# Optimization experiments

Hardware: AMD Instinct MI355X
Metric: run time of the kernel (lower is better)

Reference implementation:

```python
import jax, jax.numpy as jnp
import numpy as np

DIM, NH, HD = 1536, 12, 128          # dim, num_heads, head_dim
F, H, W = 100, 8, 8                   # video grid; F>81 triggers frame-sparse branch
L = F * H * W                         # 6400 tokens


def setup_inputs() -> dict:
    key = jax.random.key(0)
    ks = jax.random.split(key, 8)
    lin = lambda k: jax.random.normal(k, (DIM, DIM), jnp.float32) * 0.02
    return {
        "x": jax.random.normal(ks[0], (1, L, DIM), jnp.float32),
        "freqs": jax.random.uniform(ks[1], (1024, HD // 2), jnp.float32, 0.0, 2.0 * np.pi),
        "Wq": lin(ks[2]), "bq": jnp.zeros((DIM,), jnp.float32),
        "Wk": lin(ks[3]), "bk": jnp.zeros((DIM,), jnp.float32),
        "Wv": lin(ks[4]), "bv": jnp.zeros((DIM,), jnp.float32),
        "Wo": lin(ks[5]), "bo": jnp.zeros((DIM,), jnp.float32),
        "gq": jnp.ones((DIM,), jnp.float32),
        "gk": jnp.ones((DIM,), jnp.float32),
        "seq_lens": jnp.full((1,), L, jnp.int32),
        "grid_sizes": jnp.array([[F, H, W]], jnp.int32),
    }


def _rms(x, g, eps=1e-6):
    # WanRMSNorm: rms over the full channel dim, fp32 math
    m = jnp.mean(x * x, axis=-1, keepdims=True)
    return x * jax.lax.rsqrt(m + eps) * g


def _rope_tables(freqs, f, h, w):
    # freqs: [1024, c] rope angles; split c into (c-2*(c//3), c//3, c//3) for F/H/W axes
    c = freqs.shape[1]
    c1 = c - 2 * (c // 3)
    c2 = c // 3
    af = jnp.broadcast_to(freqs[:f, None, None, :c1], (f, h, w, c1))
    ah = jnp.broadcast_to(freqs[None, :h, None, c1:c1 + c2], (f, h, w, c2))
    aw = jnp.broadcast_to(freqs[None, None, :w, c1 + c2:], (f, h, w, c2))
    ang = jnp.concatenate([af, ah, aw], axis=-1).reshape(f * h * w, 1, c)  # [L,1,c]
    return jnp.cos(ang), jnp.sin(ang)


def _rope_apply(x, cos, sin):
    # x: [B,L,n,d]; pairs (real, imag) interleaved along d -> complex rotation
    b, l, n, d = x.shape
    xr, xi = x[..., 0::2], x[..., 1::2]                       # [B,L,n,c]
    out_r = xr * cos - xi * sin
    out_i = xr * sin + xi * cos
    return jnp.stack([out_r, out_i], axis=-1).reshape(b, l, n, d)


def reference(x, freqs, Wq, bq, Wk, bk, Wv, bv, Wo, bo, gq, gk, seq_lens, grid_sizes):
    b, l, _ = x.shape
    n, d = NH, HD
    f, h, w = [int(v) for v in np.asarray(grid_sizes)[0]]
    q = _rms(x @ Wq + bq, gq).reshape(b, l, n, d)
    k = _rms(x @ Wk + bk, gk).reshape(b, l, n, d)
    v = (x @ Wv + bv).reshape(b, l, n, d)
    cos, sin = _rope_tables(freqs, f, h, w)
    q = _rope_apply(q, cos, sin)
    k = _rope_apply(k, cos, sin)
    if f > 81:  # long-video frame-sparse branch: keep every 2nd frame's K/V tokens
        tpf = h * w
        idx = (jnp.arange(0, f, 2)[:, None] * tpf + jnp.arange(tpf)[None, :]).reshape(-1)
        k = k[:, idx]
        v = v[:, idx]
    # attention in low precision (original uses fp16/bf16), softmax accum fp32
    qb, kb, vb = (t.astype(jnp.bfloat16) for t in (q, k, v))
    scale = 1.0 / np.sqrt(d)
    scores = jnp.einsum('blnd,bknd->bnlk', qb, kb).astype(jnp.float32) * scale
    att = jax.nn.softmax(scores, axis=-1).astype(jnp.bfloat16)
    out = jnp.einsum('bnlk,bknd->blnd', att, vb).reshape(b, l, n * d).astype(jnp.float32)
    return out @ Wo + bo
```

## Files before the change

### kernel.cpp

```cpp
#include <hip/hip_runtime.h>
#include <stdint.h>

typedef unsigned short u16;
typedef short short8 __attribute__((ext_vector_type(8)));
typedef float f32x4 __attribute__((ext_vector_type(4)));
typedef u16 u16x8 __attribute__((ext_vector_type(8)));

#define DIMN 1536
#define LQ   6400
#define LKV  3200
#define NHEAD 12
#define HDIM  128

__device__ __forceinline__ u16 f2bf(float f) {
  uint32_t u = __builtin_bit_cast(uint32_t, f);
  u += 0x7fffu + ((u >> 16) & 1u);
  return (u16)(u >> 16);
}
__device__ __forceinline__ float bf2f(u16 h) {
  uint32_t u = ((uint32_t)h) << 16;
  return __builtin_bit_cast(float, u);
}
__device__ __forceinline__ void async16(const void* g, void* l) {
  __builtin_amdgcn_global_load_lds((const __attribute__((address_space(1))) void*)g,
                                   (__attribute__((address_space(3))) void*)l, 16, 0, 0);
}
#define MFMA16(a, b, c) __builtin_amdgcn_mfma_f32_16x16x32_bf16((a), (b), (c), 0, 0, 0)

__global__ void __launch_bounds__(256) convert_x(const float* __restrict__ x, u16* __restrict__ xb) {
  size_t i = ((size_t)blockIdx.x * 256 + threadIdx.x) * 4;
  float4 v = *(const float4*)(x + i);
  union { u16 h[4]; uint2 u; } p;
  p.h[0] = f2bf(v.x); p.h[1] = f2bf(v.y); p.h[2] = f2bf(v.z); p.h[3] = f2bf(v.w);
  *(uint2*)(xb + i) = p.u;
}

__global__ void __launch_bounds__(256) transpose_w(const float* __restrict__ Wq, const float* __restrict__ Wk,
                                                   const float* __restrict__ Wv, const float* __restrict__ Wo,
                                                   u16* __restrict__ wt) {
  int z = blockIdx.z;
  const float* W = (z == 0) ? Wq : (z == 1) ? Wk : (z == 2) ? Wv : Wo;
  u16* dst = wt + (size_t)z * DIMN * DIMN;
  __shared__ float tile[64][65];
  int c0 = blockIdx.x * 64, r0 = blockIdx.y * 64;
  int t = threadIdx.x;
  int rr = t >> 4, cc = (t & 15) * 4;
#pragma unroll
  for (int j = 0; j < 4; j++) {
    float4 v = *(const float4*)(W + (size_t)(r0 + rr + j * 16) * DIMN + c0 + cc);
    tile[rr + j * 16][cc + 0] = v.x; tile[rr + j * 16][cc + 1] = v.y;
    tile[rr + j * 16][cc + 2] = v.z; tile[rr + j * 16][cc + 3] = v.w;
  }
  __syncthreads();
  int nn = t >> 2, kk = (t & 3) * 16;
  u16x8 a, b;
#pragma unroll
  for (int q = 0; q < 8; q++) a[q] = f2bf(tile[kk + q][nn]);
#pragma unroll
  for (int q = 0; q < 8; q++) b[q] = f2bf(tile[kk + 8 + q][nn]);
  u16* o = dst + (size_t)(c0 + nn) * DIMN + r0 + kk;
  *(u16x8*)(o) = a;
  *(u16x8*)(o + 8) = b;
}

__device__ __forceinline__ void gemm_tile(const u16* __restrict__ A, const u16* __restrict__ Bt,
                                          int m0, int n0, u16* sA, u16* sB, f32x4 acc[4][4]) {
  const int tid = threadIdx.x;
  const int wid = tid >> 6, lane = tid & 63;
  const int wm = wid >> 1, wn = wid & 1;
  const int l15 = lane & 15, quad = lane >> 4;
  const int lrow = lane >> 3;
  const int sgrp = (lane & 7) ^ lrow;
#pragma unroll
  for (int i = 0; i < 4; i++)
#pragma unroll
    for (int j = 0; j < 4; j++) acc[i][j] = f32x4{0.f, 0.f, 0.f, 0.f};
  const u16* ga = A  + (size_t)(m0 + wid * 32 + lrow) * DIMN + sgrp * 8;
  const u16* gb = Bt + (size_t)(n0 + wid * 32 + lrow) * DIMN + sgrp * 8;
  u16* la = sA + (wid * 32) * 64;
  u16* lb = sB + (wid * 32) * 64;
  const int swz = l15 & 7;
  for (int k0 = 0; k0 < DIMN; k0 += 64) {
    __syncthreads();
#pragma unroll
    for (int j = 0; j < 4; j++) async16(ga + k0 + j * 8 * DIMN, la + j * 8 * 64);
#pragma unroll
    for (int j = 0; j < 4; j++) async16(gb + k0 + j * 8 * DIMN, lb + j * 8 * 64);
    __syncthreads();
#pragma unroll
    for (int kk = 0; kk < 64; kk += 32) {
      short8 af[4], bf[4];
#pragma unroll
      for (int s = 0; s < 4; s++)
        af[s] = *(const short8*)(sA + (wm * 64 + s * 16 + l15) * 64 + ((((kk >> 3) + quad) ^ swz) << 3));
#pragma unroll
      for (int s = 0; s < 4; s++)
        bf[s] = *(const short8*)(sB + (wn * 64 + s * 16 + l15) * 64 + ((((kk >> 3) + quad) ^ swz) << 3));
#pragma unroll
      for (int i = 0; i < 4; i++)
#pragma unroll
        for (int j = 0; j < 4; j++) acc[i][j] = MFMA16(af[i], bf[j], acc[i][j]);
    }
  }
}

__global__ void __launch_bounds__(256) gemm_qkv(const u16* __restrict__ xb, const u16* __restrict__ wt,
                                                const float* __restrict__ bq, const float* __restrict__ bk,
                                                const float* __restrict__ bv,
                                                u16* __restrict__ qb, u16* __restrict__ kb, u16* __restrict__ vtb) {
  __shared__ u16 sA[128 * 64];
  __shared__ u16 sB[128 * 64];
  int z = blockIdx.z;
  const u16* Bt = wt + (size_t)z * DIMN * DIMN;
  int m0 = blockIdx.x * 128, n0 = blockIdx.y * 128;
  f32x4 acc[4][4];
  gemm_tile(xb, Bt, m0, n0, sA, sB, acc);
  const float* bias = (z == 0) ? bq : (z == 1) ? bk : bv;
  int tid = threadIdx.x, wid = tid >> 6, lane = tid & 63;
  int wm = wid >> 1, wn = wid & 1, l15 = lane & 15, quad = lane >> 4;
#pragma unroll
  for (int sn = 0; sn < 4; sn++) {
    int c = n0 + wn * 64 + sn * 16 + l15;
    float bb = bias[c];
    int h = c >> 7, d = c & 127;
#pragma unroll
    for (int sm = 0; sm < 4; sm++) {
      int rl = wm * 64 + sm * 16 + quad * 4;
#pragma unroll
      for (int r = 0; r < 4; r++) {
        float val = acc[sm][sn][r] + bb;
        int row = m0 + rl + r;
        if (z == 0) {
          qb[((size_t)h * LQ + row) * HDIM + d] = f2bf(val);
        } else if ((rl + r) < 64) {
          int lk = (row >> 7) * 64 + (row & 63);
          if (z == 1) kb[((size_t)h * LKV + lk) * HDIM + d] = f2bf(val);
          else        vtb[((size_t)h * HDIM + d) * LKV + lk] = f2bf(val);
        }
      }
    }
  }
}

__global__ void __launch_bounds__(256) rms_rope(u16* __restrict__ qb, u16* __restrict__ kb,
                                                const float* __restrict__ freqs,
                                                const float* __restrict__ gq, const float* __restrict__ gk) {
  int t = blockIdx.x * 4 + (threadIdx.x >> 6);
  int lane = threadIdx.x & 63;
  bool isQ = t < LQ;
  int tok = isQ ? t : t - LQ;
  int Lt = isQ ? LQ : LKV;
  u16* buf = isQ ? qb : kb;
  const float* g = isQ ? gq : gk;
  int l = isQ ? tok : ((tok >> 6) * 128 + (tok & 63));
  float a[12], b[12];
  float ss = 0.f;
#pragma unroll
  for (int n = 0; n < NHEAD; n++) {
    ushort2 p = *(const ushort2*)(buf + ((size_t)n * Lt + tok) * HDIM + 2 * lane);
    a[n] = bf2f(p.x); b[n] = bf2f(p.y);
    ss += a[n] * a[n] + b[n] * b[n];
  }
#pragma unroll
  for (int off = 32; off; off >>= 1) ss += __shfl_xor(ss, off);
  float rs = rsqrtf(ss * (1.0f / 1536.0f) + 1e-6f);
  int i = lane;
  int fi = (i < 22) ? (l >> 6) : (i < 43) ? ((l >> 3) & 7) : (l & 7);
  float ang = freqs[fi * 64 + i];
  float sn, cs;
  sincosf(ang, &sn, &cs);
#pragma unroll
  for (int n = 0; n < NHEAD; n++) {
    float2 gg = *(const float2*)(g + n * HDIM + 2 * lane);
    float xr = a[n] * rs * gg.x;
    float xi = b[n] * rs * gg.y;
    ushort2 o;
    o.x = f2bf(xr * cs - xi * sn);
    o.y = f2bf(xr * sn + xi * cs);
    *(ushort2*)(buf + ((size_t)n * Lt + tok) * HDIM + 2 * lane) = o;
  }
}

__global__ void __launch_bounds__(256, 2) attn(const u16* __restrict__ qb, const u16* __restrict__ kb,
                                               const u16* __restrict__ vtb, u16* __restrict__ ob) {
  __shared__ u16 Ks[128 * 128];
  __shared__ u16 Vs[128 * 128];
  int x8 = blockIdx.x & 7, gsl = blockIdx.x >> 3;
  int w = x8 * 75 + gsl;
  int h = w / 50, qt = w % 50;
  int tid = threadIdx.x, wid = tid >> 6, lane = tid & 63;
  int l15 = lane & 15, quad = lane >> 4;
  int l0 = qt * 128;
  short8 qf[2][4];
#pragma unroll
  for (int mf = 0; mf < 2; mf++)
#pragma unroll
    for (int ks = 0; ks < 4; ks++)
      qf[mf][ks] = *(const short8*)(qb + ((size_t)h * LQ + l0 + wid * 32 + mf * 16 + l15) * HDIM + ks * 32 + quad * 8);
  f32x4 O[2][8];
#pragma unroll
  for (int mf = 0; mf < 2; mf++)
#pragma unroll
    for (int d = 0; d < 8; d++) O[mf][d] = f32x4{0.f, 0.f, 0.f, 0.f};
  float m_[2][4], l_[2][4];
#pragma unroll
  for (int mf = 0; mf < 2; mf++)
#pragma unroll
    for (int r = 0; r < 4; r++) { m_[mf][r] = -3e38f; l_[mf][r] = 0.f; }
  const float scale = 0.08838834764831845f;
  const u16* kg = kb + (size_t)h * LKV * HDIM;
  const u16* vg = vtb + (size_t)h * HDIM * LKV;
  for (int kb0 = 0; kb0 < LKV; kb0 += 128) {
    __syncthreads();
#pragma unroll
    for (int j = 0; j < 8; j++) {
      int row = wid * 32 + j * 4 + quad;
      int cg = (l15 ^ ((j * 4 + quad) & 15)) * 8;
      async16(kg + (size_t)(kb0 + row) * HDIM + cg, Ks + (wid * 32 + j * 4) * 128);
      async16(vg + (size_t)row * LKV + kb0 + cg, Vs + (wid * 32 + j * 4) * 128);
    }
    __syncthreads();
    f32x4 S[2][8];
#pragma unroll
    for (int nt = 0; nt < 8; nt++) {
      f32x4 s0 = f32x4{0.f, 0.f, 0.f, 0.f}, s1 = f32x4{0.f, 0.f, 0.f, 0.f};
#pragma unroll
      for (int ks = 0; ks < 4; ks++) {
        short8 kf = *(const short8*)(Ks + (nt * 16 + l15) * 128 + (((ks * 4 + quad) ^ l15) << 3));
        s0 = MFMA16(qf[0][ks], kf, s0);
        s1 = MFMA16(qf[1][ks], kf, s1);
      }
      S[0][nt] = s0; S[1][nt] = s1;
    }
    float al[2][4];
#pragma unroll
    for (int mf = 0; mf < 2; mf++)
#pragma unroll
      for (int r = 0; r < 4; r++) {
        float mx = S[mf][0][r];
#pragma unroll
        for (int nt = 1; nt < 8; nt++) mx = fmaxf(mx, S[mf][nt][r]);
#pragma unroll
        for (int off = 1; off < 16; off <<= 1) mx = fmaxf(mx, __shfl_xor(mx, off));
        float mn = fmaxf(m_[mf][r], mx);
        al[mf][r] = __expf((m_[mf][r] - mn) * scale);
        m_[mf][r] = mn;
        float sum = 0.f;
#pragma unroll
        for (int nt = 0; nt < 8; nt++) {
          float p = __expf((S[mf][nt][r] - mn) * scale);
          S[mf][nt][r] = p;
          sum += p;
        }
#pragma unroll
        for (int off = 1; off < 16; off <<= 1) sum += __shfl_xor(sum, off);
        l_[mf][r] = l_[mf][r] * al[mf][r] + sum;
      }
    __syncthreads();
#pragma unroll
    for (int mf = 0; mf < 2; mf++)
#pragma unroll
      for (int nt = 0; nt < 8; nt++)
#pragma unroll
        for (int r = 0; r < 4; r++) {
          int row = wid * 32 + mf * 16 + quad * 4 + r;
          int grp = (nt * 2 + (l15 >> 3)) ^ (quad * 4 + r);
          Ks[row * 128 + grp * 8 + (l15 & 7)] = f2bf(S[mf][nt][r]);
        }
#pragma unroll
    for (int mf = 0; mf < 2; mf++)
#pragma unroll
      for (int d = 0; d < 8; d++) {
        f32x4 o = O[mf][d];
#pragma unroll
        for (int r = 0; r < 4; r++) o[r] *= al[mf][r];
        O[mf][d] = o;
      }
#pragma unroll
    for (int ks = 0; ks < 4; ks++) {
      int sw = ((ks * 4 + quad) ^ l15) << 3;
      short8 pf0 = *(const short8*)(Ks + (wid * 32 + l15) * 128 + sw);
      short8 pf1 = *(const short8*)(Ks + (wid * 32 + 16 + l15) * 128 + sw);
#pragma unroll
      for (int d = 0; d < 8; d++) {
        short8 vf = *(const short8*)(Vs + (d * 16 + l15) * 128 + sw);
        O[0][d] = MFMA16(pf0, vf, O[0][d]);
        O[1][d] = MFMA16(pf1, vf, O[1][d]);
      }
    }
  }
  float inv[2][4];
#pragma unroll
  for (int mf = 0; mf < 2; mf++)
#pragma unroll
    for (int r = 0; r < 4; r++) inv[mf][r] = 1.0f / l_[mf][r];
#pragma unroll
  for (int mf = 0; mf < 2; mf++)
#pragma unroll
    for (int d = 0; d < 8; d++)
#pragma unroll
      for (int r = 0; r < 4; r++) {
        int row = l0 + wid * 32 + mf * 16 + quad * 4 + r;
        int col = h * HDIM + d * 16 + l15;
        ob[(size_t)row * DIMN + col] = f2bf(O[mf][d][r] * inv[mf][r]);
      }
}

__global__ void __launch_bounds__(256) gemm_out(const u16* __restrict__ ob, const u16* __restrict__ wto,
                                                const float* __restrict__ bo, float* __restrict__ out) {
  __shared__ u16 sA[128 * 64];
  __shared__ u16 sB[128 * 64];
  int m0 = blockIdx.x * 128, n0 = blockIdx.y * 128;
  f32x4 acc[4][4];
  gemm_tile(ob, wto, m0, n0, sA, sB, acc);
  int tid = threadIdx.x, wid = tid >> 6, lane = tid & 63;
  int wm = wid >> 1, wn = wid & 1, l15 = lane & 15, quad = lane >> 4;
#pragma unroll
  for (int sn = 0; sn < 4; sn++) {
    int c = n0 + wn * 64 + sn * 16 + l15;
    float bb = bo[c];
#pragma unroll
    for (int sm = 0; sm < 4; sm++) {
      int rl = wm * 64 + sm * 16 + quad * 4;
#pragma unroll
      for (int r = 0; r < 4; r++)
        out[(size_t)(m0 + rl + r) * DIMN + c] = acc[sm][sn][r] + bb;
    }
  }
}

extern "C" void kernel_launch(void* const* d_in, const int* in_sizes, int n_in,
                              void* d_out, int out_size, void* d_ws, size_t ws_size,
                              hipStream_t stream) {
  (void)in_sizes; (void)n_in; (void)out_size; (void)ws_size;
  const float* x     = (const float*)d_in[0];
  const float* freqs = (const float*)d_in[1];
  const float* Wq    = (const float*)d_in[2];
  const float* bq    = (const float*)d_in[3];
  const float* Wk    = (const float*)d_in[4];
  const float* bk    = (const float*)d_in[5];
  const float* Wv    = (const float*)d_in[6];
  const float* bv    = (const float*)d_in[7];
  const float* Wo    = (const float*)d_in[8];
  const float* bo    = (const float*)d_in[9];
  const float* gq    = (const float*)d_in[10];
  const float* gk    = (const float*)d_in[11];

  u16* xb  = (u16*)d_ws;
  u16* wt  = xb  + (size_t)LQ * DIMN;
  u16* qb  = wt  + (size_t)4 * DIMN * DIMN;
  u16* kb  = qb  + (size_t)NHEAD * LQ * HDIM;
  u16* vtb = kb  + (size_t)NHEAD * LKV * HDIM;
  u16* ob  = vtb + (size_t)NHEAD * HDIM * LKV;

  convert_x<<<dim3(9600), dim3(256), 0, stream>>>(x, xb);
  transpose_w<<<dim3(24, 24, 4), dim3(256), 0, stream>>>(Wq, Wk, Wv, Wo, wt);
  gemm_qkv<<<dim3(50, 12, 3), dim3(256), 0, stream>>>(xb, wt, bq, bk, bv, qb, kb, vtb);
  rms_rope<<<dim3(2400), dim3(256), 0, stream>>>(qb, kb, freqs, gq, gk);
  attn<<<dim3(600), dim3(256), 0, stream>>>(qb, kb, vtb, ob);
  gemm_out<<<dim3(50, 12), dim3(256), 0, stream>>>(ob, wt + (size_t)3 * DIMN * DIMN, bo, (float*)d_out);
}
```

Measured before the change: 788.3 us.

## Load K/V fragments directly from global memory in attention, drop shared staging

New measurement: 1.252 ms. +58.9%, slower.

```diff
diff --git a/kernel.cpp b/kernel.cpp
--- a/kernel.cpp
+++ b/kernel.cpp
@@ -181,22 +181,22 @@
   }
 }
 
-__global__ void __launch_bounds__(256, 2) attn(const u16* __restrict__ qb, const u16* __restrict__ kb,
+__global__ void __launch_bounds__(128, 3) attn(const u16* __restrict__ qb, const u16* __restrict__ kb,
                                                const u16* __restrict__ vtb, u16* __restrict__ ob) {
-  __shared__ u16 Ks[128 * 128];
-  __shared__ u16 Vs[128 * 128];
+  __shared__ u16 Ps[2][32 * 128];
   int x8 = blockIdx.x & 7, gsl = blockIdx.x >> 3;
-  int w = x8 * 75 + gsl;
-  int h = w / 50, qt = w % 50;
+  int w = x8 * 150 + gsl;
+  int h = w / 100, qt = w % 100;
   int tid = threadIdx.x, wid = tid >> 6, lane = tid & 63;
   int l15 = lane & 15, quad = lane >> 4;
-  int l0 = qt * 128;
+  int l0 = qt * 64 + wid * 32;
+  u16* ps = Ps[wid];
   short8 qf[2][4];
 #pragma unroll
   for (int mf = 0; mf < 2; mf++)
 #pragma unroll
     for (int ks = 0; ks < 4; ks++)
-      qf[mf][ks] = *(const short8*)(qb + ((size_t)h * LQ + l0 + wid * 32 + mf * 16 + l15) * HDIM + ks * 32 + quad * 8);
+      qf[mf][ks] = *(const short8*)(qb + ((size_t)h * LQ + l0 + mf * 16 + l15) * HDIM + ks * 32 + quad * 8);
   f32x4 O[2][8];
 #pragma unroll
   for (int mf = 0; mf < 2; mf++)
@@ -208,27 +208,21 @@
 #pragma unroll
     for (int r = 0; r < 4; r++) { m_[mf][r] = -3e38f; l_[mf][r] = 0.f; }
   const float scale = 0.08838834764831845f;
-  const u16* kg = kb + (size_t)h * LKV * HDIM;
-  const u16* vg = vtb + (size_t)h * HDIM * LKV;
+  const u16* kgl = kb  + (size_t)h * LKV * HDIM + (size_t)l15 * HDIM + quad * 8;
+  const u16* vgl = vtb + (size_t)h * HDIM * LKV + (size_t)l15 * LKV + quad * 8;
   for (int kb0 = 0; kb0 < LKV; kb0 += 128) {
-    __syncthreads();
-#pragma unroll
-    for (int j = 0; j < 8; j++) {
-      int row = wid * 32 + j * 4 + quad;
-      int cg = (l15 ^ ((j * 4 + quad) & 15)) * 8;
-      async16(kg + (size_t)(kb0 + row) * HDIM + cg, Ks + (wid * 32 + j * 4) * 128);
-      async16(vg + (size_t)row * LKV + kb0 + cg, Vs + (wid * 32 + j * 4) * 128);
-    }
-    __syncthreads();
     f32x4 S[2][8];
 #pragma unroll
     for (int nt = 0; nt < 8; nt++) {
+      short8 kf[4];
+#pragma unroll
+      for (int ks = 0; ks < 4; ks++)
+        kf[ks] = *(const short8*)(kgl + (size_t)(kb0 + nt * 16) * HDIM + ks * 32);
       f32x4 s0 = f32x4{0.f, 0.f, 0.f, 0.f}, s1 = f32x4{0.f, 0.f, 0.f, 0.f};
 #pragma unroll
       for (int ks = 0; ks < 4; ks++) {
-        short8 kf = *(const short8*)(Ks + (nt * 16 + l15) * 128 + (((ks * 4 + quad) ^ l15) << 3));
-        s0 = MFMA16(qf[0][ks], kf, s0);
-        s1 = MFMA16(qf[1][ks], kf, s1);
+        s0 = MFMA16(qf[0][ks], kf[ks], s0);
+        s1 = MFMA16(qf[1][ks], kf[ks], s1);
       }
       S[0][nt] = s0; S[1][nt] = s1;
     }
@@ -256,16 +250,15 @@
         for (int off = 1; off < 16; off <<= 1) sum += __shfl_xor(sum, off);
         l_[mf][r] = l_[mf][r] * al[mf][r] + sum;
       }
-    __syncthreads();
 #pragma unroll
     for (int mf = 0; mf < 2; mf++)
 #pragma unroll
       for (int nt = 0; nt < 8; nt++)
 #pragma unroll
         for (int r = 0; r < 4; r++) {
-          int row = wid * 32 + mf * 16 + quad * 4 + r;
-          int grp = (nt * 2 + (l15 >> 3)) ^ (quad * 4 + r);
-          Ks[row * 128 + grp * 8 + (l15 & 7)] = f2bf(S[mf][nt][r]);
+          int rw = mf * 16 + quad * 4 + r;
+          int grp = (nt * 2 + (l15 >> 3)) ^ (rw & 15);
+          ps[rw * 128 + grp * 8 + (l15 & 7)] = f2bf(S[mf][nt][r]);
         }
 #pragma unroll
     for (int mf = 0; mf < 2; mf++)
@@ -279,13 +272,13 @@
 #pragma unroll
     for (int ks = 0; ks < 4; ks++) {
       int sw = ((ks * 4 + quad) ^ l15) << 3;
-      short8 pf0 = *(const short8*)(Ks + (wid * 32 + l15) * 128 + sw);
-      short8 pf1 = *(const short8*)(Ks + (wid * 32 + 16 + l15) * 128 + sw);
-#pragma unroll
-      for (int d = 0; d < 8; d++) {
-        short8 vf = *(const short8*)(Vs + (d * 16 + l15) * 128 + sw);
-        O[0][d] = MFMA16(pf0, vf, O[0][d]);
-        O[1][d] = MFMA16(pf1, vf, O[1][d]);
+      short8 pf0 = *(const short8*)(ps + l15 * 128 + sw);
+      short8 pf1 = *(const short8*)(ps + (16 + l15) * 128 + sw);
+#pragma unroll
+      for (int dt = 0; dt < 8; dt++) {
+        short8 vf = *(const short8*)(vgl + (size_t)dt * 16 * LKV + kb0 + ks * 32);
+        O[0][dt] = MFMA16(pf0, vf, O[0][dt]);
+        O[1][dt] = MFMA16(pf1, vf, O[1][dt]);
       }
     }
   }
@@ -300,7 +293,7 @@
     for (int d = 0; d < 8; d++)
 #pragma unroll
       for (int r = 0; r < 4; r++) {
-        int row = l0 + wid * 32 + mf * 16 + quad * 4 + r;
+        int row = l0 + mf * 16 + quad * 4 + r;
         int col = h * HDIM + d * 16 + l15;
         ob[(size_t)row * DIMN + col] = f2bf(O[mf][d][r] * inv[mf][r]);
       }
@@ -357,6 +350,6 @@
   transpose_w<<<dim3(24, 24, 4), dim3(256), 0, stream>>>(Wq, Wk, Wv, Wo, wt);
   gemm_qkv<<<dim3(50, 12, 3), dim3(256), 0, stream>>>(xb, wt, bq, bk, bv, qb, kb, vtb);
   rms_rope<<<dim3(2400), dim3(256), 0, stream>>>(qb, kb, freqs, gq, gk);
-  attn<<<dim3(600), dim3(256), 0, stream>>>(qb, kb, vtb, ob);
+  attn<<<dim3(1200), dim3(128), 0, stream>>>(qb, kb, vtb, ob);
   gemm_out<<<dim3(50, 12), dim3(256), 0, stream>>>(ob, wt + (size_t)3 * DIMN * DIMN, bo, (float*)d_out);
 }
```
